# Kernel optimization log

Measured on AMD Instinct MI355X. Metric: run time of the kernel, lower is better.

The kernel has to match this reference:

```python
import jax, jax.numpy as jnp
import numpy as np

N = 20000      # n_nodes
E = 320000     # n_edges (multiple of 4, so _from_coo drops nothing)
D = 512        # embed_dim
H = 8          # num_heads
DK = D // H    # d_k = 64


def setup_inputs() -> dict:
    key = jax.random.key(0)
    ks = jax.random.split(key, 12)
    x = jax.random.normal(ks[0], (N, D), jnp.float32)
    rows = jnp.sort(jax.random.randint(ks[1], (E,), 0, N))
    cols = jax.random.randint(ks[2], (E,), 0, N)
    edge_index = jnp.stack([rows, cols]).astype(jnp.int32)  # [2, E]
    att_bias = jax.random.normal(ks[3], (E, H), jnp.float32)
    s = float(1.0 / np.sqrt(D))  # ~xavier scale
    Wq = jax.random.normal(ks[4], (D, D), jnp.float32) * s
    Wk = jax.random.normal(ks[5], (D, D), jnp.float32) * s
    Wv = jax.random.normal(ks[6], (D, D), jnp.float32) * s
    Wo = jax.random.normal(ks[7], (D, D), jnp.float32) * s
    bq = jnp.zeros((D,), jnp.float32)
    bk = jnp.zeros((D,), jnp.float32)
    bv = jnp.zeros((D,), jnp.float32)
    bo = jnp.zeros((D,), jnp.float32)
    return dict(x=x, edge_index=edge_index, att_bias=att_bias,
                Wq=Wq, bq=bq, Wk=Wk, bk=bk, Wv=Wv, bv=bv, Wo=Wo, bo=bo)


def reference(x, edge_index, att_bias, Wq, bq, Wk, bk, Wv, bv, Wo, bo):
    n = x.shape[0]
    rows, cols = edge_index[0], edge_index[1]
    # per-head projections: [n, H, DK]
    q = (x @ Wq + bq).reshape(n, H, DK)
    k = (x @ Wk + bk).reshape(n, H, DK)
    v = (x @ Wv + bv).reshape(n, H, DK)
    scale = 1.0 / jnp.sqrt(jnp.asarray(DK, x.dtype))
    # masked QK^T on the edge pattern, plus additive bias: [E, H]
    logits = jnp.einsum('ehd,ehd->eh', q[rows] * scale, k[cols]) + att_bias
    # CSR (segment) softmax over each destination row
    row_max = jax.ops.segment_max(logits, rows, num_segments=n)      # [n, H]
    p = jnp.exp(logits - row_max[rows])                              # [E, H]
    denom = jax.ops.segment_sum(p, rows, num_segments=n)            # [n, H]
    att = p / denom[rows]                                            # [E, H]
    # sparse-dense bmm: y[i] = sum_{e: rows[e]=i} att[e] * v[cols[e]]
    y = jax.ops.segment_sum(att[:, :, None] * v[cols], rows, num_segments=n)  # [n, H, DK]
    out = y.reshape(n, H * DK) @ Wo + bo
    return out
```

## Files before the change

kernel.cpp:

```cpp
#include <hip/hip_runtime.h>
#include <hip/hip_bf16.h>

typedef unsigned short ushort_t;
typedef unsigned int uint32;
typedef __attribute__((ext_vector_type(8))) short short8;
typedef __attribute__((ext_vector_type(4))) float floatx4;

#define DEV __device__ __forceinline__

DEV float b2f(ushort_t u) { return __uint_as_float(((uint32)u) << 16); }
DEV ushort_t f2b(float f) {
  __hip_bfloat16 h = __float2bfloat16(f);
  return __builtin_bit_cast(unsigned short, h);
}
DEV void unpack8(const uint4& u, float* f) {
  f[0] = __uint_as_float(u.x << 16); f[1] = __uint_as_float(u.x & 0xffff0000u);
  f[2] = __uint_as_float(u.y << 16); f[3] = __uint_as_float(u.y & 0xffff0000u);
  f[4] = __uint_as_float(u.z << 16); f[5] = __uint_as_float(u.z & 0xffff0000u);
  f[6] = __uint_as_float(u.w << 16); f[7] = __uint_as_float(u.w & 0xffff0000u);
}

__global__ __launch_bounds__(256) void k_detect(const ushort_t* __restrict__ x,
                                                int* __restrict__ flag) {
  __shared__ int red[256];
  int tid = threadIdx.x;
  int wild = 0;
  for (int i = tid; i < 4096; i += 256) {
    uint32 e = (x[i] >> 7) & 0xFFu;
    if (e < 100u || e > 140u) wild++;
  }
  red[tid] = wild;
  __syncthreads();
  for (int s = 128; s > 0; s >>= 1) {
    if (tid < s) red[tid] += red[tid + s];
    __syncthreads();
  }
  if (tid == 0) flag[0] = (red[0] > 400) ? 1 : 0;
}

__global__ __launch_bounds__(256) void k_transpose(
    const void* __restrict__ Wq, const void* __restrict__ Wk,
    const void* __restrict__ Wv, const void* __restrict__ Wo,
    ushort_t* __restrict__ WT4, const int* __restrict__ flagp) {
  __shared__ ushort_t t[32][33];
  int isf32 = *flagp;
  int z = blockIdx.z;
  const void* src = (z == 0) ? Wq : (z == 1) ? Wk : (z == 2) ? Wv : Wo;
  ushort_t* dst = WT4 + (size_t)z * 512 * 512;
  int bx = blockIdx.x, by = blockIdx.y;
  int tx = threadIdx.x, ty = threadIdx.y;
#pragma unroll
  for (int i = 0; i < 4; i++) {
    size_t idx = (size_t)(by * 32 + ty + 8 * i) * 512 + bx * 32 + tx;
    ushort_t v = isf32 ? f2b(((const float*)src)[idx]) : ((const ushort_t*)src)[idx];
    t[ty + 8 * i][tx] = v;
  }
  __syncthreads();
#pragma unroll
  for (int i = 0; i < 4; i++)
    dst[(size_t)(bx * 32 + ty + 8 * i) * 512 + by * 32 + tx] = t[tx][ty + 8 * i];
}

__global__ __launch_bounds__(256) void k_biases(
    const void* __restrict__ bq, const void* __restrict__ bk,
    const void* __restrict__ bv, const void* __restrict__ bo,
    float* __restrict__ biasf, const int* __restrict__ flagp) {
  int i = blockIdx.x * 256 + threadIdx.x;
  if (i >= 2048) return;
  int z = i >> 9, j = i & 511;
  const void* b = (z == 0) ? bq : (z == 1) ? bk : (z == 2) ? bv : bo;
  biasf[i] = (*flagp) ? ((const float*)b)[j] : b2f(((const ushort_t*)b)[j]);
}

__global__ __launch_bounds__(256) void k_convx(
    const void* __restrict__ x, ushort_t* __restrict__ xb, int n8,
    const int* __restrict__ flagp) {
  int i = blockIdx.x * 256 + threadIdx.x;
  if (i >= n8) return;
  if (*flagp) {
    const float* xf = (const float*)x + (size_t)i * 8;
    float4 f0 = ((const float4*)xf)[0];
    float4 f1 = ((const float4*)xf)[1];
    uint4 o;
    o.x = (uint32)f2b(f0.x) | ((uint32)f2b(f0.y) << 16);
    o.y = (uint32)f2b(f0.z) | ((uint32)f2b(f0.w) << 16);
    o.z = (uint32)f2b(f1.x) | ((uint32)f2b(f1.y) << 16);
    o.w = (uint32)f2b(f1.z) | ((uint32)f2b(f1.w) << 16);
    ((uint4*)xb)[i] = o;
  } else {
    ((uint4*)xb)[i] = ((const uint4*)x)[i];
  }
}

__global__ void k_build_rp(const int* __restrict__ rows, int E, int N, int* __restrict__ rp) {
  int i = blockIdx.x * blockDim.x + threadIdx.x;
  if (i > N) return;
  int lo = 0, hi = E;
  while (lo < hi) {
    int mid = (lo + hi) >> 1;
    if (rows[mid] < i) lo = mid + 1; else hi = mid;
  }
  rp[i] = lo;
}

DEV void gemm_body(const ushort_t* __restrict__ A, const ushort_t* __restrict__ BT,
                   const float* __restrict__ bias, void* C,
                   int M, int ldc, float scale, int row0, int by, int f32out) {
  __shared__ ushort_t As[128 * 32];
  __shared__ ushort_t Bs[128 * 32];
  int tid = threadIdx.x;
  int w = tid >> 6, lane = tid & 63;

  int u0 = tid, u1 = tid + 256;
  int sr0 = u0 >> 2, sk0 = (u0 & 3) * 8;
  int sr1 = u1 >> 2, sk1 = (u1 & 3) * 8;
  const int nG0 = by * 128;

  floatx4 acc[4][4];
#pragma unroll
  for (int i = 0; i < 4; i++)
#pragma unroll
    for (int j = 0; j < 4; j++)
#pragma unroll
      for (int r = 0; r < 4; r++) acc[i][j][r] = 0.f;

  int lm = lane & 15, quad = lane >> 4;
  int wr = w >> 1, wc = w & 1;

  int rA0 = row0 + sr0; if (rA0 >= M) rA0 = M - 1;
  int rA1 = row0 + sr1; if (rA1 >= M) rA1 = M - 1;

  for (int k0 = 0; k0 < 512; k0 += 32) {
    uint4 a0 = *(const uint4*)(A + (size_t)rA0 * 512 + k0 + sk0);
    uint4 a1 = *(const uint4*)(A + (size_t)rA1 * 512 + k0 + sk1);
    uint4 b0 = *(const uint4*)(BT + (size_t)(nG0 + sr0) * 512 + k0 + sk0);
    uint4 b1 = *(const uint4*)(BT + (size_t)(nG0 + sr1) * 512 + k0 + sk1);
    __syncthreads();
    *(uint4*)(As + sr0 * 32 + sk0) = a0;
    *(uint4*)(As + sr1 * 32 + sk1) = a1;
    *(uint4*)(Bs + sr0 * 32 + sk0) = b0;
    *(uint4*)(Bs + sr1 * 32 + sk1) = b1;
    __syncthreads();

    const ushort_t* pa = As + (wr * 64 + lm) * 32 + quad * 8;
    const ushort_t* pb = Bs + (wc * 64 + lm) * 32 + quad * 8;
    short8 af[4], bfr[4];
#pragma unroll
    for (int t4 = 0; t4 < 4; t4++) {
      af[t4]  = *(const short8*)(pa + t4 * 16 * 32);
      bfr[t4] = *(const short8*)(pb + t4 * 16 * 32);
    }
#pragma unroll
    for (int mt = 0; mt < 4; mt++)
#pragma unroll
      for (int nt = 0; nt < 4; nt++)
        acc[mt][nt] = __builtin_amdgcn_mfma_f32_16x16x32_bf16(af[mt], bfr[nt], acc[mt][nt], 0, 0, 0);
  }

  int colB = by * 128 + wc * 64 + lm;
  float bv4[4];
#pragma unroll
  for (int nt = 0; nt < 4; nt++) bv4[nt] = bias[colB + nt * 16];
#pragma unroll
  for (int mt = 0; mt < 4; mt++) {
    int rg0 = row0 + wr * 64 + mt * 16 + quad * 4;
#pragma unroll
    for (int nt = 0; nt < 4; nt++) {
#pragma unroll
      for (int r = 0; r < 4; r++) {
        int rg = rg0 + r;
        if (rg < M) {
          float val = (acc[mt][nt][r] + bv4[nt]) * scale;
          size_t off = (size_t)rg * ldc + colB + nt * 16;
          if (f32out) ((float*)C)[off] = val;
          else        ((ushort_t*)C)[off] = f2b(val);
        }
      }
    }
  }
}

__global__ __launch_bounds__(256) void k_gemm_qkv(
    const ushort_t* __restrict__ xb, const ushort_t* __restrict__ WT4,
    const float* __restrict__ biasf, ushort_t* Qp, ushort_t* KV, int M) {
  int z = blockIdx.z;
  const ushort_t* BT = WT4 + (size_t)z * 512 * 512;
  const float* bias = biasf + (size_t)z * 512;
  ushort_t* Cp = (z == 0) ? Qp : (z == 1) ? KV : (KV + 512);
  int ldc = (z == 0) ? 512 : 1024;
  float scale = (z == 0) ? 0.125f : 1.0f;
  gemm_body(xb, BT, bias, Cp, M, ldc, scale, blockIdx.x * 128, blockIdx.y, 0);
}

__global__ __launch_bounds__(256) void k_gemm_out(
    const ushort_t* __restrict__ y, const ushort_t* __restrict__ WT4,
    const float* __restrict__ biasf, void* out, int M,
    const int* __restrict__ flagp) {
  gemm_body(y, WT4 + (size_t)3 * 512 * 512, biasf + 3 * 512, out, M, 512, 1.0f,
            blockIdx.x * 128, blockIdx.y, *flagp);
}

__global__ __launch_bounds__(256) void k_edge(
    ushort_t* Qy, const ushort_t* __restrict__ KV,
    const void* __restrict__ ab, const int* __restrict__ cols,
    const int* __restrict__ rp, int Nn, int E, const int* __restrict__ flagp) {
  int node = blockIdx.x * 4 + (threadIdx.x >> 6);
  if (node >= Nn) return;
  int lane = threadIdx.x & 63;
  int h8 = lane >> 3;
  int isf32 = *flagp;

  uint4 qu = ((const uint4*)(Qy + (size_t)node * 512))[lane];
  float qf[8];
  unpack8(qu, qf);

  int e0 = rp[node], e1 = rp[node + 1];
  if (e0 < 0) e0 = 0;
  if (e1 > E) e1 = E;

  float m = -__builtin_inff(), s = 0.f;
  float accv[8];
#pragma unroll
  for (int j = 0; j < 8; j++) accv[j] = 0.f;

  for (int e = e0; e < e1; ++e) {
    int c = cols[e];
    const ushort_t* kvrow = KV + (size_t)c * 1024;
    uint4 ku = ((const uint4*)kvrow)[lane];
    uint4 vu = ((const uint4*)(kvrow + 512))[lane];
    float kf[8];
    unpack8(ku, kf);
    float d = 0.f;
#pragma unroll
    for (int j = 0; j < 8; j++) d = fmaf(qf[j], kf[j], d);
    d += __shfl_xor(d, 1);
    d += __shfl_xor(d, 2);
    d += __shfl_xor(d, 4);
    size_t bi = (size_t)e * 8 + h8;
    float logit = d + (isf32 ? ((const float*)ab)[bi] : b2f(((const ushort_t*)ab)[bi]));
    float mn = fmaxf(m, logit);
    float alpha = __expf(m - mn);
    float pw = __expf(logit - mn);
    s = s * alpha + pw;
    float vf[8];
    unpack8(vu, vf);
#pragma unroll
    for (int j = 0; j < 8; j++) accv[j] = accv[j] * alpha + pw * vf[j];
    m = mn;
  }

  float inv = (e1 > e0 && s > 0.f) ? 1.f / s : 0.f;
  ushort_t hb[8];
#pragma unroll
  for (int j = 0; j < 8; j++) hb[j] = f2b(accv[j] * inv);
  uint4 uh;
  uh.x = (uint32)hb[0] | ((uint32)hb[1] << 16);
  uh.y = (uint32)hb[2] | ((uint32)hb[3] << 16);
  uh.z = (uint32)hb[4] | ((uint32)hb[5] << 16);
  uh.w = (uint32)hb[6] | ((uint32)hb[7] << 16);
  ((uint4*)(Qy + (size_t)node * 512))[lane] = uh;
}

extern "C" void kernel_launch(void* const* d_in, const int* in_sizes, int n_in,
                              void* d_out, int out_size, void* d_ws, size_t ws_size,
                              hipStream_t stream) {
  const void* x  = d_in[0];
  const int* ei  = (const int*)d_in[1];
  const void* ab = d_in[2];
  const void* Wq = d_in[3];
  const void* bq = d_in[4];
  const void* Wk = d_in[5];
  const void* bk = d_in[6];
  const void* Wv = d_in[7];
  const void* bv = d_in[8];
  const void* Wo = d_in[9];
  const void* bo = d_in[10];

  const int D = 512;
  int M = in_sizes[0] / D;
  int E = in_sizes[1] / 2;
  const int* rows = ei;
  const int* cols = ei + E;

  char* p = (char*)d_ws;
  size_t off = 0;
  auto carve = [&](size_t bytes) -> void* {
    off = (off + 255) & ~(size_t)255;
    void* r = p + off;
    off += bytes;
    return r;
  };
  int* flag      = (int*)carve(4);
  ushort_t* WT4  = (ushort_t*)carve((size_t)4 * 512 * 512 * 2);
  float* biasf   = (float*)carve((size_t)4 * 512 * 4);
  ushort_t* xb   = (ushort_t*)carve((size_t)M * 512 * 2);
  ushort_t* Qp   = (ushort_t*)carve((size_t)M * 512 * 2);
  ushort_t* KV   = (ushort_t*)carve((size_t)M * 1024 * 2);
  int* rp        = (int*)carve((size_t)(M + 1) * 4);
  (void)ws_size;

  k_detect<<<1, 256, 0, stream>>>((const ushort_t*)x, flag);
  k_transpose<<<dim3(16, 16, 4), dim3(32, 8), 0, stream>>>(Wq, Wk, Wv, Wo, WT4, flag);
  k_biases<<<8, 256, 0, stream>>>(bq, bk, bv, bo, biasf, flag);
  int n8 = M * 512 / 8;
  k_convx<<<(n8 + 255) / 256, 256, 0, stream>>>(x, xb, n8, flag);
  k_build_rp<<<(M + 1 + 255) / 256, 256, 0, stream>>>(rows, E, M, rp);

  int rb = (M + 127) / 128;
  k_gemm_qkv<<<dim3(rb, 4, 3), 256, 0, stream>>>(xb, WT4, biasf, Qp, KV, M);
  k_edge<<<(M + 3) / 4, 256, 0, stream>>>(Qp, KV, ab, cols, rp, M, E, flag);
  k_gemm_out<<<dim3(rb, 4, 1), 256, 0, stream>>>(Qp, WT4, biasf, d_out, M, flag);
}
```

Baseline: 317.3 us.

## Use direct global-to-LDS loads in GEMM and prefetch next edge in attention

The GEMM tile loads now use global_load_lds to write directly into shared memory instead of staging through registers, with per-wave row assignment and an extra barrier after the MFMA loop. The edge-attention loop software-pipelines the K/V row gathers and bias load one edge ahead so memory latency overlaps the compute. This trades register staging for async copies and adds registers for the prefetched data. The global_load_lds layout assumes contiguous 16-byte per-lane placement, which matches the 32-element row stride.

```diff
diff --git a/kernel.cpp b/kernel.cpp
--- a/kernel.cpp
+++ b/kernel.cpp
@@ -19,6 +19,10 @@
   f[4] = __uint_as_float(u.z << 16); f[5] = __uint_as_float(u.z & 0xffff0000u);
   f[6] = __uint_as_float(u.w << 16); f[7] = __uint_as_float(u.w & 0xffff0000u);
 }
+
+#define GLOAD_LDS(gp, lp) \
+  __builtin_amdgcn_global_load_lds((const __attribute__((address_space(1))) uint32*)(gp), \
+                                   (__attribute__((address_space(3))) uint32*)(lp), 16, 0, 0)
 
 __global__ __launch_bounds__(256) void k_detect(const ushort_t* __restrict__ x,
                                                 int* __restrict__ flag) {
@@ -110,11 +114,8 @@
   __shared__ ushort_t Bs[128 * 32];
   int tid = threadIdx.x;
   int w = tid >> 6, lane = tid & 63;
-
-  int u0 = tid, u1 = tid + 256;
-  int sr0 = u0 >> 2, sk0 = (u0 & 3) * 8;
-  int sr1 = u1 >> 2, sk1 = (u1 & 3) * 8;
-  const int nG0 = by * 128;
+  int sr = lane >> 2;
+  int sk = (lane & 3) * 8;
 
   floatx4 acc[4][4];
 #pragma unroll
@@ -126,20 +127,20 @@
 
   int lm = lane & 15, quad = lane >> 4;
   int wr = w >> 1, wc = w & 1;
-
-  int rA0 = row0 + sr0; if (rA0 >= M) rA0 = M - 1;
-  int rA1 = row0 + sr1; if (rA1 >= M) rA1 = M - 1;
+  const int nG = by * 128 + w * 32;
+
+  int rA0 = row0 + w * 32 + sr; if (rA0 >= M) rA0 = M - 1;
+  int rA1 = rA0 + 16;          if (rA1 >= M) rA1 = M - 1;
+  const ushort_t* gA0 = A + (size_t)rA0 * 512 + sk;
+  const ushort_t* gA1 = A + (size_t)rA1 * 512 + sk;
+  const ushort_t* gB0 = BT + (size_t)(nG + sr) * 512 + sk;
+  const ushort_t* gB1 = BT + (size_t)(nG + 16 + sr) * 512 + sk;
 
   for (int k0 = 0; k0 < 512; k0 += 32) {
-    uint4 a0 = *(const uint4*)(A + (size_t)rA0 * 512 + k0 + sk0);
-    uint4 a1 = *(const uint4*)(A + (size_t)rA1 * 512 + k0 + sk1);
-    uint4 b0 = *(const uint4*)(BT + (size_t)(nG0 + sr0) * 512 + k0 + sk0);
-    uint4 b1 = *(const uint4*)(BT + (size_t)(nG0 + sr1) * 512 + k0 + sk1);
-    __syncthreads();
-    *(uint4*)(As + sr0 * 32 + sk0) = a0;
-    *(uint4*)(As + sr1 * 32 + sk1) = a1;
-    *(uint4*)(Bs + sr0 * 32 + sk0) = b0;
-    *(uint4*)(Bs + sr1 * 32 + sk1) = b1;
+    GLOAD_LDS(gA0 + k0, As + (w * 32 + 0) * 32);
+    GLOAD_LDS(gA1 + k0, As + (w * 32 + 16) * 32);
+    GLOAD_LDS(gB0 + k0, Bs + (w * 32 + 0) * 32);
+    GLOAD_LDS(gB1 + k0, Bs + (w * 32 + 16) * 32);
     __syncthreads();
 
     const ushort_t* pa = As + (wr * 64 + lm) * 32 + quad * 8;
@@ -155,6 +156,7 @@
 #pragma unroll
       for (int nt = 0; nt < 4; nt++)
         acc[mt][nt] = __builtin_amdgcn_mfma_f32_16x16x32_bf16(af[mt], bfr[nt], acc[mt][nt], 0, 0, 0);
+    __syncthreads();
   }
 
   int colB = by * 128 + wc * 64 + lm;
@@ -223,30 +225,45 @@
 #pragma unroll
   for (int j = 0; j < 8; j++) accv[j] = 0.f;
 
+  uint4 ku0, vu0, ku1, vu1;
+  float ab0, ab1;
+  if (e0 < e1) {
+    int c = cols[e0];
+    const ushort_t* kvrow = KV + (size_t)c * 1024;
+    ku0 = ((const uint4*)kvrow)[lane];
+    vu0 = ((const uint4*)(kvrow + 512))[lane];
+    size_t bi = (size_t)e0 * 8 + h8;
+    ab0 = isf32 ? ((const float*)ab)[bi] : b2f(((const ushort_t*)ab)[bi]);
+  }
+
   for (int e = e0; e < e1; ++e) {
-    int c = cols[e];
-    const ushort_t* kvrow = KV + (size_t)c * 1024;
-    uint4 ku = ((const uint4*)kvrow)[lane];
-    uint4 vu = ((const uint4*)(kvrow + 512))[lane];
+    if (e + 1 < e1) {
+      int c = cols[e + 1];
+      const ushort_t* kvrow = KV + (size_t)c * 1024;
+      ku1 = ((const uint4*)kvrow)[lane];
+      vu1 = ((const uint4*)(kvrow + 512))[lane];
+      size_t bi = (size_t)(e + 1) * 8 + h8;
+      ab1 = isf32 ? ((const float*)ab)[bi] : b2f(((const ushort_t*)ab)[bi]);
+    }
     float kf[8];
-    unpack8(ku, kf);
+    unpack8(ku0, kf);
     float d = 0.f;
 #pragma unroll
     for (int j = 0; j < 8; j++) d = fmaf(qf[j], kf[j], d);
     d += __shfl_xor(d, 1);
     d += __shfl_xor(d, 2);
     d += __shfl_xor(d, 4);
-    size_t bi = (size_t)e * 8 + h8;
-    float logit = d + (isf32 ? ((const float*)ab)[bi] : b2f(((const ushort_t*)ab)[bi]));
+    float logit = d + ab0;
     float mn = fmaxf(m, logit);
     float alpha = __expf(m - mn);
     float pw = __expf(logit - mn);
     s = s * alpha + pw;
     float vf[8];
-    unpack8(vu, vf);
+    unpack8(vu0, vf);
 #pragma unroll
     for (int j = 0; j < 8; j++) accv[j] = accv[j] * alpha + pw * vf[j];
     m = mn;
+    ku0 = ku1; vu0 = vu1; ab0 = ab1;
   }
 
   float inv = (e1 > e0 && s > 0.f) ? 1.f / s : 0.f;
```

Result: no change. 313.6 us (-1.2%).
